# Performance work log

Hardware: AMD Instinct MI355X
Metric: run time of the kernel (lower is better)

## Reference

```python
import jax, jax.numpy as jnp
import numpy as np

B, T, DIM, H, KV, HD = 1, 2048, 2048, 16, 4, 128


def _rope_tables(T, hd):
    half = hd // 2
    inv_freq = 1.0 / (10000.0 ** (np.arange(0, half, dtype=np.float32) / half))
    t = np.arange(T, dtype=np.float32)
    freqs = np.outer(t, inv_freq)                # [T, hd/2]
    emb = np.concatenate([freqs, freqs], axis=-1)  # [T, hd]
    return jnp.asarray(np.cos(emb)), jnp.asarray(np.sin(emb))


def setup_inputs() -> dict:
    key = jax.random.key(0)
    kx, kq, kk, kv, ko = jax.random.split(key, 5)
    s = 0.02
    x = jax.random.normal(kx, (B, T, DIM), dtype=jnp.float32)
    wq = jax.random.normal(kq, (H * HD, DIM), dtype=jnp.float32) * s
    wk = jax.random.normal(kk, (KV * HD, DIM), dtype=jnp.float32) * s
    wv = jax.random.normal(kv, (KV * HD, DIM), dtype=jnp.float32) * s
    wo = jax.random.normal(ko, (DIM, H * HD), dtype=jnp.float32) * s
    cos, sin = _rope_tables(T, HD)
    return {"x": x, "wq": wq, "wk": wk, "wv": wv, "wo": wo, "cos": cos, "sin": sin}


def _rotate_half(u):
    u1, u2 = jnp.split(u, 2, axis=-1)
    return jnp.concatenate([-u2, u1], axis=-1)


def _apply_rope(u, cos, sin):
    # u: [B, T, h, hd]; cos/sin: [T, hd]
    c = cos[None, :, None, :]
    s = sin[None, :, None, :]
    return u * c + _rotate_half(u) * s


def reference(x, wq, wk, wv, wo, cos, sin):
    b, t, dim = x.shape
    hd = cos.shape[1]
    h = wq.shape[0] // hd
    kvh = wk.shape[0] // hd
    rep = h // kvh
    scale = hd ** -0.5

    q = (x @ wq.T).reshape(b, t, h, hd)
    k = (x @ wk.T).reshape(b, t, kvh, hd)
    v = (x @ wv.T).reshape(b, t, kvh, hd)

    q = _apply_rope(q, cos, sin)
    k = _apply_rope(k, cos, sin)

    # Group queries by shared KV head instead of materializing repeat_kv
    qg = q.reshape(b, t, kvh, rep, hd)
    scores = jnp.einsum('bqgrd,bkgd->bgrqk', qg, k) * scale  # [b,g,r,T,T]
    causal = jnp.tril(jnp.ones((t, t), dtype=bool))
    scores = jnp.where(causal[None, None, None], scores, jnp.float32(-1e30))
    attn = jax.nn.softmax(scores, axis=-1)
    out = jnp.einsum('bgrqk,bkgd->bqgrd', attn, v).reshape(b, t, h * hd)
    return out @ wo.T
```

## Files before the change

kernel.cpp:

```cpp
#include <hip/hip_runtime.h>
#include <hip/hip_bf16.h>

typedef unsigned short u16;
typedef __attribute__((ext_vector_type(8))) short bf16x8;
typedef __attribute__((ext_vector_type(4))) float f32x4;

#define T_SEQ 2048
#define DIM   2048
#define NH    16
#define NKV   4
#define HD    128
#define NQKV  3072
#define SCALE 0.08838834764831845f
#define NSLOT 61

__device__ __forceinline__ u16 f2bf(float f) {
  unsigned int u = __float_as_uint(f);
  unsigned int r = (u + 0x7fffu + ((u >> 16) & 1u)) >> 16;
  return (u16)r;
}
__device__ __forceinline__ float bf2f(u16 v) {
  return __uint_as_float(((unsigned int)v) << 16);
}
__device__ __forceinline__ void gload_lds16(const u16* g, u16* l) {
  __builtin_amdgcn_global_load_lds(
      (const __attribute__((address_space(1))) unsigned int*)g,
      (__attribute__((address_space(3))) unsigned int*)l, 16, 0, 0);
}

#define C1 1048576
#define C2 2097152
#define C3 2359296
#define C4 2621440
__global__ void cast_main(const float4* __restrict__ x,  const float4* __restrict__ wq,
                          const float4* __restrict__ wk, const float4* __restrict__ wv,
                          ushort4* __restrict__ xb, ushort4* __restrict__ wqkvb) {
  int i = blockIdx.x * 256 + threadIdx.x;
  const float4* src; ushort4* dst; int j;
  if (i < C1)      { src = x;  dst = xb;               j = i; }
  else if (i < C2) { src = wq; dst = wqkvb;            j = i - C1; }
  else if (i < C3) { src = wk; dst = wqkvb + 1048576;  j = i - C2; }
  else             { src = wv; dst = wqkvb + 1310720;  j = i - C3; }
  float4 v = src[j];
  ushort4 o;
  o.x = f2bf(v.x); o.y = f2bf(v.y); o.z = f2bf(v.z); o.w = f2bf(v.w);
  dst[j] = o;
}
__global__ void cast_wo(const float4* __restrict__ wo, ushort4* __restrict__ wob) {
  int i = blockIdx.x * 256 + threadIdx.x;
  float4 v = wo[i];
  ushort4 o;
  o.x = f2bf(v.x); o.y = f2bf(v.y); o.z = f2bf(v.z); o.w = f2bf(v.w);
  wob[i] = o;
}

#define BM 128
#define BN 128
#define BK 64

__global__ __launch_bounds__(256) void gemm_bt(
    const u16* __restrict__ A, const u16* __restrict__ W,
    float* __restrict__ Cf, u16* __restrict__ Cb, int M, int N, int K)
{
  __shared__ u16 As[BM * BK];
  __shared__ u16 Bs[BN * BK];
  const int tid  = threadIdx.x;
  const int lane = tid & 63;
  const int wave = tid >> 6;
  const int ln   = lane & 15;
  const int quad = lane >> 4;
  const int m0 = blockIdx.y * BM;
  const int n0 = blockIdx.x * BN;
  const int wm = (wave >> 1) * 64;
  const int wn = (wave & 1) * 64;

  const int srow = wave * 32 + (lane >> 3);
  const int scol = (lane & 7) * 8;
  const u16* ga = A + (size_t)(m0 + srow) * K + scol;
  const u16* gw = W + (size_t)(n0 + srow) * K + scol;
  u16* la = &As[wave * 32 * BK];
  u16* lb = &Bs[wave * 32 * BK];

  f32x4 acc[4][4] = {};

  for (int k0 = 0; k0 < K; k0 += BK) {
#pragma unroll
    for (int i = 0; i < 4; ++i) {
      gload_lds16(ga + k0 + (size_t)(i * 8) * K, la + i * 8 * BK);
      gload_lds16(gw + k0 + (size_t)(i * 8) * K, lb + i * 8 * BK);
    }
    __syncthreads();
#pragma unroll
    for (int ks = 0; ks < 2; ++ks) {
      bf16x8 af[4], bfr[4];
#pragma unroll
      for (int mt = 0; mt < 4; ++mt)
        af[mt] = *(const bf16x8*)&As[(wm + mt * 16 + ln) * BK + ks * 32 + quad * 8];
#pragma unroll
      for (int nt = 0; nt < 4; ++nt)
        bfr[nt] = *(const bf16x8*)&Bs[(wn + nt * 16 + ln) * BK + ks * 32 + quad * 8];
#pragma unroll
      for (int mt = 0; mt < 4; ++mt)
#pragma unroll
        for (int nt = 0; nt < 4; ++nt)
          acc[mt][nt] = __builtin_amdgcn_mfma_f32_16x16x32_bf16(
              af[mt], bfr[nt], acc[mt][nt], 0, 0, 0);
    }
    __syncthreads();
  }

#pragma unroll
  for (int mt = 0; mt < 4; ++mt)
#pragma unroll
    for (int nt = 0; nt < 4; ++nt)
#pragma unroll
      for (int r = 0; r < 4; ++r) {
        int row = m0 + wm + mt * 16 + quad * 4 + r;
        int col = n0 + wn + nt * 16 + ln;
        if (Cb) Cb[(size_t)row * N + col] = f2bf(acc[mt][nt][r]);
        else    Cf[(size_t)row * N + col] = acc[mt][nt][r];
      }
}

__global__ void rope_fused(const u16* __restrict__ QKVb,
                           const float* __restrict__ cosT,
                           const float* __restrict__ sinT,
                           u16* __restrict__ Qs, u16* __restrict__ Kb,
                           u16* __restrict__ Vt)
{
  int b = blockIdx.x, d = threadIdx.x;
  if (b < T_SEQ * NH) {
    int t = b >> 4;
    int h = b & 15;
    const u16* row = QKVb + (size_t)t * NQKV + h * HD;
    float u = bf2f(row[d]);
    float pr = (d < 64) ? -bf2f(row[d + 64]) : bf2f(row[d - 64]);
    float c = cosT[t * HD + d], s = sinT[t * HD + d];
    Qs[(size_t)b * HD + d] = f2bf((u * c + pr * s) * SCALE);
  } else if (b < T_SEQ * (NH + NKV)) {
    int b2 = b - T_SEQ * NH;
    int t = b2 >> 2;
    int g = b2 & 3;
    const u16* row = QKVb + (size_t)t * NQKV + DIM + g * HD;
    float u = bf2f(row[d]);
    float pr = (d < 64) ? -bf2f(row[d + 64]) : bf2f(row[d - 64]);
    float c = cosT[t * HD + d], s = sinT[t * HD + d];
    Kb[(size_t)b2 * HD + d] = f2bf(u * c + pr * s);
  } else {
    int b3 = b - T_SEQ * (NH + NKV);
    int idx = b3 * 128 + d;
    int t  = idx & (T_SEQ - 1);
    int dd = (idx >> 11) & (HD - 1);
    int g  = idx >> 18;
    Vt[idx] = QKVb[(size_t)t * NQKV + DIM + NKV * HD + g * HD + dd];
  }
}

__global__ __launch_bounds__(256) void flash_partial(
    const u16* __restrict__ Qs, const u16* __restrict__ Kb,
    const u16* __restrict__ Vt, u16* __restrict__ Opart,
    float* __restrict__ lpart)
{
  __shared__ u16 Ks[64 * 128];
  __shared__ u16 Vs[128 * 64];
  __shared__ u16 Ps[4][16 * 64];

  const int srev = 60 - (int)blockIdx.x;
  const int h = blockIdx.y;
  int qi, c;
  if      (srev >= 54) { qi = 15; c = srev - 54; }
  else if (srev >= 48) { qi = 14; c = srev - 48; }
  else if (srev >= 42) { qi = 13; c = srev - 42; }
  else if (srev >= 36) { qi = 12; c = srev - 36; }
  else if (srev >= 31) { qi = 11; c = srev - 31; }
  else if (srev >= 26) { qi = 10; c = srev - 26; }
  else if (srev >= 22) { qi = 9;  c = srev - 22; }
  else if (srev >= 18) { qi = 8;  c = srev - 18; }
  else if (srev >= 14) { qi = 7;  c = srev - 14; }
  else if (srev >= 11) { qi = 6;  c = srev - 11; }
  else if (srev >= 8)  { qi = 5;  c = srev - 8; }
  else if (srev >= 6)  { qi = 4;  c = srev - 6; }
  else if (srev >= 4)  { qi = 3;  c = srev - 4; }
  else if (srev >= 2)  { qi = 2;  c = srev - 2; }
  else                 { qi = srev; c = 0; }

  const int nt   = 2 * (qi + 1);
  const int nc   = (2 * qi + 6) / 5;
  const int tb   = nt / nc, rem = nt % nc;
  const int t0   = c * tb + (c < rem ? c : rem);
  const int tcnt = tb + (c < rem ? 1 : 0);
  const int g  = h >> 2;
  const int q0 = qi << 7;

  const int tid  = threadIdx.x;
  const int lane = tid & 63;
  const int w    = tid >> 6;
  const int ln   = lane & 15;
  const int quad = lane >> 4;
  const int lx   = ln & 7;

  bf16x8 aq[2][4];
#pragma unroll
  for (int mt = 0; mt < 2; ++mt) {
    const u16* qp = Qs + ((size_t)(q0 + w * 32 + mt * 16 + ln) * NH + h) * HD + quad * 8;
#pragma unroll
    for (int ks = 0; ks < 4; ++ks) aq[mt][ks] = *(const bf16x8*)&qp[ks * 32];
  }

  f32x4 o[2][8] = {};
  float rs[2][4] = {};

  for (int it = t0; it < t0 + tcnt; ++it) {
    const int jb = it << 6;
    {
      int r = tid >> 4, ch = tid & 15;
#pragma unroll
      for (int i = 0; i < 4; ++i) {
        int row = i * 16 + r;
        *(bf16x8*)&Ks[row * 128 + ((ch ^ (row & 7)) << 3)] =
            *(const bf16x8*)&Kb[((size_t)(jb + row) * NKV + g) * HD + ch * 8];
      }
    }
    {
      int r = tid >> 3, ch = tid & 7;
#pragma unroll
      for (int i = 0; i < 4; ++i) {
        int row = i * 32 + r;
        *(bf16x8*)&Vs[row * 64 + ((ch ^ (row & 7)) << 3)] =
            *(const bf16x8*)&Vt[(size_t)(g * HD + row) * T_SEQ + jb + ch * 8];
      }
    }
    __syncthreads();

#pragma unroll
    for (int mt = 0; mt < 2; ++mt) {
      const int rbase = q0 + w * 32 + mt * 16 + quad * 4;
      const int rmax  = q0 + w * 32 + mt * 16 + 15;
      if (jb <= rmax) {
        f32x4 sc[4];
#pragma unroll
        for (int nb = 0; nb < 4; ++nb) {
          f32x4 s = {};
#pragma unroll
          for (int ks = 0; ks < 4; ++ks) {
            bf16x8 kf = *(const bf16x8*)&Ks[(nb * 16 + ln) * 128 +
                                            ((((ks << 2) + quad) ^ lx) << 3)];
            s = __builtin_amdgcn_mfma_f32_16x16x32_bf16(aq[mt][ks], kf, s, 0, 0, 0);
          }
          sc[nb] = s;
        }
        const bool diag = (jb >= q0);
#pragma unroll
        for (int nb = 0; nb < 4; ++nb) {
          int j = jb + nb * 16 + ln;
#pragma unroll
          for (int r = 0; r < 4; ++r) {
            float p = (!diag || j <= rbase + r) ? __expf(sc[nb][r]) : 0.f;
            rs[mt][r] += p;
            int prow = quad * 4 + r;
            Ps[w][prow * 64 + ((((nb << 1) + (ln >> 3)) ^ (prow & 7)) << 3) + (ln & 7)] = f2bf(p);
          }
        }
#pragma unroll
        for (int kst = 0; kst < 2; ++kst) {
          bf16x8 ap = *(const bf16x8*)&Ps[w][ln * 64 + ((((kst << 2) + quad) ^ lx) << 3)];
#pragma unroll
          for (int nb8 = 0; nb8 < 8; ++nb8) {
            bf16x8 bv = *(const bf16x8*)&Vs[(nb8 * 16 + ln) * 64 +
                                            ((((kst << 2) + quad) ^ lx) << 3)];
            o[mt][nb8] = __builtin_amdgcn_mfma_f32_16x16x32_bf16(ap, bv, o[mt][nb8], 0, 0, 0);
          }
        }
      }
    }
    __syncthreads();
  }

  const int slot = h * NSLOT + srev;
  u16*   op = Opart + (size_t)slot * (128 * 128);
  float* lp = lpart + (size_t)slot * 128;
#pragma unroll
  for (int mt = 0; mt < 2; ++mt) {
#pragma unroll
    for (int r = 0; r < 4; ++r)
#pragma unroll
      for (int off = 1; off < 16; off <<= 1)
        rs[mt][r] += __shfl_xor(rs[mt][r], off);
    int rowb = w * 32 + mt * 16 + quad * 4;
#pragma unroll
    for (int r = 0; r < 4; ++r) {
#pragma unroll
      for (int nb8 = 0; nb8 < 8; ++nb8)
        op[(rowb + r) * 128 + nb8 * 16 + ln] = f2bf(o[mt][nb8][r]);
      if (ln == 0) lp[rowb + r] = rs[mt][r];
    }
  }
}

__global__ void flash_reduce(const u16* __restrict__ Opart,
                             const float* __restrict__ lpart,
                             u16* __restrict__ AO)
{
  const int h = blockIdx.y;
  const int d = threadIdx.x & 127;
  const int t = blockIdx.x * 2 + (threadIdx.x >> 7);
  const int qi = t >> 7, r = t & 127;
  int p = 0;
#pragma unroll
  for (int j = 0; j < 16; ++j) p += (j < qi) ? ((2 * j + 6) / 5) : 0;
  const int nc = (2 * qi + 6) / 5;
  const int base = h * NSLOT + p;
  float so = 0.f, sl = 0.f;
  for (int cc = 0; cc < nc; ++cc) {
    so += bf2f(Opart[(size_t)(base + cc) * (128 * 128) + r * 128 + d]);
    sl += lpart[(size_t)(base + cc) * 128 + r];
  }
  AO[(size_t)t * DIM + h * HD + d] = f2bf(so / sl);
}

extern "C" void kernel_launch(void* const* d_in, const int* in_sizes, int n_in,
                              void* d_out, int out_size, void* d_ws, size_t ws_size,
                              hipStream_t stream) {
  const float* x    = (const float*)d_in[0];
  const float* wq   = (const float*)d_in[1];
  const float* wk   = (const float*)d_in[2];
  const float* wv   = (const float*)d_in[3];
  const float* wo   = (const float*)d_in[4];
  const float* cosT = (const float*)d_in[5];
  const float* sinT = (const float*)d_in[6];
  float* out = (float*)d_out;

  char* ws = (char*)d_ws;
  const size_t MB = 1024 * 1024;
  u16*   xb    = (u16*)(ws + 0 * MB);
  u16*   wqkvb = (u16*)(ws + 8 * MB);
  u16*   QKVb  = (u16*)(ws + 20 * MB);
  u16*   wob   = (u16*)(ws + 0 * MB);
  u16*   Qs    = (u16*)(ws + 8 * MB);
  u16*   Kb    = (u16*)(ws + 16 * MB);
  u16*   Vt    = (u16*)(ws + 18 * MB);
  u16*   Opart = (u16*)(ws + 20 * MB);
  float* lpart = (float*)(ws + 51 * MB);
  u16*   AO    = (u16*)(ws + 8 * MB);

  cast_main<<<C4 / 256, 256, 0, stream>>>(
      (const float4*)x, (const float4*)wq, (const float4*)wk, (const float4*)wv,
      (ushort4*)xb, (ushort4*)wqkvb);

  gemm_bt<<<dim3(NQKV / BN, T_SEQ / BM), 256, 0, stream>>>(
      xb, wqkvb, nullptr, QKVb, T_SEQ, NQKV, DIM);

  cast_wo<<<(DIM * DIM / 4) / 256, 256, 0, stream>>>((const float4*)wo, (ushort4*)wob);

  rope_fused<<<T_SEQ * (NH + NKV) + (NKV * HD * T_SEQ) / 128, HD, 0, stream>>>(
      QKVb, cosT, sinT, Qs, Kb, Vt);

  flash_partial<<<dim3(NSLOT, NH), 256, 0, stream>>>(Qs, Kb, Vt, Opart, lpart);
  flash_reduce<<<dim3(T_SEQ / 2, NH), 256, 0, stream>>>(Opart, lpart, AO);

  gemm_bt<<<dim3(DIM / BN, T_SEQ / BM), 256, 0, stream>>>(
      AO, wob, out, nullptr, T_SEQ, DIM, DIM);
}
```

Before: 291.1 us.

## Split-K both GEMMs into two halves with bf16 partials reduced downstream

```diff
diff --git a/kernel.cpp b/kernel.cpp
--- a/kernel.cpp
+++ b/kernel.cpp
@@ -60,7 +60,8 @@
 
 __global__ __launch_bounds__(256) void gemm_bt(
     const u16* __restrict__ A, const u16* __restrict__ W,
-    float* __restrict__ Cf, u16* __restrict__ Cb, int M, int N, int K)
+    float* __restrict__ Cf, u16* __restrict__ Cb,
+    int M, int N, int Kstride, int Krun)
 {
   __shared__ u16 As[BM * BK];
   __shared__ u16 Bs[BN * BK];
@@ -71,23 +72,24 @@
   const int quad = lane >> 4;
   const int m0 = blockIdx.y * BM;
   const int n0 = blockIdx.x * BN;
+  const int koff = blockIdx.z * Krun;
   const int wm = (wave >> 1) * 64;
   const int wn = (wave & 1) * 64;
 
   const int srow = wave * 32 + (lane >> 3);
   const int scol = (lane & 7) * 8;
-  const u16* ga = A + (size_t)(m0 + srow) * K + scol;
-  const u16* gw = W + (size_t)(n0 + srow) * K + scol;
+  const u16* ga = A + (size_t)(m0 + srow) * Kstride + koff + scol;
+  const u16* gw = W + (size_t)(n0 + srow) * Kstride + koff + scol;
   u16* la = &As[wave * 32 * BK];
   u16* lb = &Bs[wave * 32 * BK];
 
   f32x4 acc[4][4] = {};
 
-  for (int k0 = 0; k0 < K; k0 += BK) {
+  for (int k0 = 0; k0 < Krun; k0 += BK) {
 #pragma unroll
     for (int i = 0; i < 4; ++i) {
-      gload_lds16(ga + k0 + (size_t)(i * 8) * K, la + i * 8 * BK);
-      gload_lds16(gw + k0 + (size_t)(i * 8) * K, lb + i * 8 * BK);
+      gload_lds16(ga + k0 + (size_t)(i * 8) * Kstride, la + i * 8 * BK);
+      gload_lds16(gw + k0 + (size_t)(i * 8) * Kstride, lb + i * 8 * BK);
     }
     __syncthreads();
 #pragma unroll
@@ -109,6 +111,7 @@
     __syncthreads();
   }
 
+  const size_t zoff = (size_t)blockIdx.z * M * N;
 #pragma unroll
   for (int mt = 0; mt < 4; ++mt)
 #pragma unroll
@@ -117,33 +120,39 @@
       for (int r = 0; r < 4; ++r) {
         int row = m0 + wm + mt * 16 + quad * 4 + r;
         int col = n0 + wn + nt * 16 + ln;
-        if (Cb) Cb[(size_t)row * N + col] = f2bf(acc[mt][nt][r]);
-        else    Cf[(size_t)row * N + col] = acc[mt][nt][r];
+        if (Cb) Cb[zoff + (size_t)row * N + col] = f2bf(acc[mt][nt][r]);
+        else    Cf[zoff + (size_t)row * N + col] = acc[mt][nt][r];
       }
 }
 
-__global__ void rope_fused(const u16* __restrict__ QKVb,
+__global__ void rope_fused(const u16* __restrict__ QKVp,
                            const float* __restrict__ cosT,
                            const float* __restrict__ sinT,
                            u16* __restrict__ Qs, u16* __restrict__ Kb,
                            u16* __restrict__ Vt)
 {
+  const u16* p0 = QKVp;
+  const u16* p1 = QKVp + (size_t)T_SEQ * NQKV;
   int b = blockIdx.x, d = threadIdx.x;
   if (b < T_SEQ * NH) {
     int t = b >> 4;
     int h = b & 15;
-    const u16* row = QKVb + (size_t)t * NQKV + h * HD;
-    float u = bf2f(row[d]);
-    float pr = (d < 64) ? -bf2f(row[d + 64]) : bf2f(row[d - 64]);
+    size_t base = (size_t)t * NQKV + h * HD;
+    float u = bf2f(p0[base + d]) + bf2f(p1[base + d]);
+    int dr = (d < 64) ? d + 64 : d - 64;
+    float pr = bf2f(p0[base + dr]) + bf2f(p1[base + dr]);
+    if (d < 64) pr = -pr;
     float c = cosT[t * HD + d], s = sinT[t * HD + d];
     Qs[(size_t)b * HD + d] = f2bf((u * c + pr * s) * SCALE);
   } else if (b < T_SEQ * (NH + NKV)) {
     int b2 = b - T_SEQ * NH;
     int t = b2 >> 2;
     int g = b2 & 3;
-    const u16* row = QKVb + (size_t)t * NQKV + DIM + g * HD;
-    float u = bf2f(row[d]);
-    float pr = (d < 64) ? -bf2f(row[d + 64]) : bf2f(row[d - 64]);
+    size_t base = (size_t)t * NQKV + DIM + g * HD;
+    float u = bf2f(p0[base + d]) + bf2f(p1[base + d]);
+    int dr = (d < 64) ? d + 64 : d - 64;
+    float pr = bf2f(p0[base + dr]) + bf2f(p1[base + dr]);
+    if (d < 64) pr = -pr;
     float c = cosT[t * HD + d], s = sinT[t * HD + d];
     Kb[(size_t)b2 * HD + d] = f2bf(u * c + pr * s);
   } else {
@@ -152,7 +161,8 @@
     int t  = idx & (T_SEQ - 1);
     int dd = (idx >> 11) & (HD - 1);
     int g  = idx >> 18;
-    Vt[idx] = QKVb[(size_t)t * NQKV + DIM + NKV * HD + g * HD + dd];
+    size_t src = (size_t)t * NQKV + DIM + NKV * HD + g * HD + dd;
+    Vt[idx] = f2bf(bf2f(p0[src]) + bf2f(p1[src]));
   }
 }
 
@@ -318,6 +328,20 @@
   AO[(size_t)t * DIM + h * HD + d] = f2bf(so / sl);
 }
 
+__global__ void reduce_out(const ushort4* __restrict__ p0,
+                           const ushort4* __restrict__ p1,
+                           float4* __restrict__ out)
+{
+  int i = blockIdx.x * 256 + threadIdx.x;
+  ushort4 a = p0[i], b = p1[i];
+  float4 v;
+  v.x = bf2f(a.x) + bf2f(b.x);
+  v.y = bf2f(a.y) + bf2f(b.y);
+  v.z = bf2f(a.z) + bf2f(b.z);
+  v.w = bf2f(a.w) + bf2f(b.w);
+  out[i] = v;
+}
+
 extern "C" void kernel_launch(void* const* d_in, const int* in_sizes, int n_in,
                               void* d_out, int out_size, void* d_ws, size_t ws_size,
                               hipStream_t stream) {
@@ -334,30 +358,33 @@
   const size_t MB = 1024 * 1024;
   u16*   xb    = (u16*)(ws + 0 * MB);
   u16*   wqkvb = (u16*)(ws + 8 * MB);
-  u16*   QKVb  = (u16*)(ws + 20 * MB);
-  u16*   wob   = (u16*)(ws + 0 * MB);
-  u16*   Qs    = (u16*)(ws + 8 * MB);
-  u16*   Kb    = (u16*)(ws + 16 * MB);
-  u16*   Vt    = (u16*)(ws + 18 * MB);
+  u16*   QKVp  = (u16*)(ws + 20 * MB);
+  u16*   Qs    = (u16*)(ws + 0 * MB);
+  u16*   Kb    = (u16*)(ws + 8 * MB);
+  u16*   Vt    = (u16*)(ws + 10 * MB);
+  u16*   wob   = (u16*)(ws + 12 * MB);
   u16*   Opart = (u16*)(ws + 20 * MB);
   float* lpart = (float*)(ws + 51 * MB);
-  u16*   AO    = (u16*)(ws + 8 * MB);
+  u16*   AO    = (u16*)(ws + 0 * MB);
+  u16*   OPp   = (u16*)(ws + 20 * MB);
 
   cast_main<<<C4 / 256, 256, 0, stream>>>(
       (const float4*)x, (const float4*)wq, (const float4*)wk, (const float4*)wv,
       (ushort4*)xb, (ushort4*)wqkvb);
 
-  gemm_bt<<<dim3(NQKV / BN, T_SEQ / BM), 256, 0, stream>>>(
-      xb, wqkvb, nullptr, QKVb, T_SEQ, NQKV, DIM);
+  gemm_bt<<<dim3(NQKV / BN, T_SEQ / BM, 2), 256, 0, stream>>>(
+      xb, wqkvb, nullptr, QKVp, T_SEQ, NQKV, DIM, DIM / 2);
 
   cast_wo<<<(DIM * DIM / 4) / 256, 256, 0, stream>>>((const float4*)wo, (ushort4*)wob);
 
   rope_fused<<<T_SEQ * (NH + NKV) + (NKV * HD * T_SEQ) / 128, HD, 0, stream>>>(
-      QKVb, cosT, sinT, Qs, Kb, Vt);
+      QKVp, cosT, sinT, Qs, Kb, Vt);
 
   flash_partial<<<dim3(NSLOT, NH), 256, 0, stream>>>(Qs, Kb, Vt, Opart, lpart);
   flash_reduce<<<dim3(T_SEQ / 2, NH), 256, 0, stream>>>(Opart, lpart, AO);
 
-  gemm_bt<<<dim3(DIM / BN, T_SEQ / BM), 256, 0, stream>>>(
-      AO, wob, out, nullptr, T_SEQ, DIM, DIM);
-}
+  gemm_bt<<<dim3(DIM / BN, T_SEQ / BM, 2), 256, 0, stream>>>(
+      AO, wob, nullptr, OPp, T_SEQ, DIM, DIM, DIM / 2);
+  reduce_out<<<(DIM * DIM / 4) / 256, 256, 0, stream>>>(
+      (const ushort4*)OPp, (const ushort4*)OPp + (size_t)T_SEQ * DIM / 4, (float4*)out);
+}
```

Result: no change. 288.2 us (-1.0%).
